# Kernel tuning notes

Hardware: AMD Instinct MI355X
Metric: run time of the kernel (lower is better)

## Reference

```python
import jax, jax.numpy as jnp
import numpy as np

DIM = 2048
N_HEAD = 16

def setup_inputs() -> dict:
    key = jax.random.key(0)
    ks = jax.random.split(key, 5)
    s_in = 1.0 / np.sqrt(DIM)
    x = jax.random.normal(ks[0], (4, 2048, DIM), dtype=jnp.float32)
    W_attn = jax.random.normal(ks[1], (DIM, 3 * DIM), dtype=jnp.float32) * s_in
    b_attn = jnp.zeros((3 * DIM,), dtype=jnp.float32)
    W_proj = jax.random.normal(ks[2], (DIM, DIM), dtype=jnp.float32) * s_in
    b_proj = jnp.zeros((DIM,), dtype=jnp.float32)
    return {"x": x, "W_attn": W_attn, "b_attn": b_attn, "W_proj": W_proj, "b_proj": b_proj}

def reference(x, W_attn, b_attn, W_proj, b_proj):
    B, T, C = x.shape
    H = N_HEAD
    Dh = C // H
    qkv = x @ W_attn + b_attn              # [B,T,3C]
    q, k, v = jnp.split(qkv, 3, axis=-1)
    # [B,T,C] -> [B,H,T,Dh]
    q = q.reshape(B, T, H, Dh).transpose(0, 2, 1, 3)
    k = k.reshape(B, T, H, Dh).transpose(0, 2, 1, 3)
    v = v.reshape(B, T, H, Dh).transpose(0, 2, 1, 3)
    scale = 1.0 / jnp.sqrt(jnp.asarray(Dh, dtype=x.dtype))
    att = jnp.einsum('bhqd,bhkd->bhqk', q, k) * scale
    att = jax.nn.softmax(att, axis=-1)
    y = jnp.einsum('bhqk,bhkd->bhqd', att, v)  # [B,H,T,Dh]
    y = y.transpose(0, 2, 1, 3).reshape(B, T, C)
    y = y @ W_proj + b_proj
    return y
```

## Files before the change

kernel.cpp:

```cpp
#include <hip/hip_runtime.h>


using bhalf  = __bf16;
using bhalf8 = __attribute__((ext_vector_type(8))) __bf16;
using floatx4 = __attribute__((ext_vector_type(4))) float;

#define MFMA16(A, B, C) __builtin_amdgcn_mfma_f32_16x16x32_bf16(A, B, C, 0, 0, 0)

__device__ __forceinline__ void gload16(const void* g, void* l) {
  __builtin_amdgcn_global_load_lds(
      (const __attribute__((address_space(1))) unsigned int*)g,
      (__attribute__((address_space(3))) unsigned int*)l, 16, 0, 0);
}

constexpr int Bn = 4, Tn = 2048, Cn = 2048, Hn = 16, Dh = 128;
constexpr int Kdim = Cn;
constexpr size_t SLOT = (size_t)Hn * Tn * Dh;

__global__ __launch_bounds__(256) void cvt_x(const float* __restrict__ in,
                                             bhalf* __restrict__ out) {
  const size_t i = ((size_t)blockIdx.x * 256 + threadIdx.x) * 8;
  const float4 a = *reinterpret_cast<const float4*>(in + i);
  const float4 b = *reinterpret_cast<const float4*>(in + i + 4);
  bhalf8 v;
  v[0] = (bhalf)a.x; v[1] = (bhalf)a.y; v[2] = (bhalf)a.z; v[3] = (bhalf)a.w;
  v[4] = (bhalf)b.x; v[5] = (bhalf)b.y; v[6] = (bhalf)b.z; v[7] = (bhalf)b.w;
  *reinterpret_cast<bhalf8*>(out + i) = v;
}

__global__ __launch_bounds__(256) void transpose_cvt(const float* __restrict__ in,
                                                     bhalf* __restrict__ out,
                                                     int ldin, int ldout, int coff) {
  __shared__ unsigned short tile[64][65];
  const int c0 = blockIdx.x * 64, r0 = blockIdx.y * 64;
  const int tx = threadIdx.x & 15, ty = threadIdx.x >> 4;
#pragma unroll
  for (int i = 0; i < 4; i++) {
    const int r = ty + i * 16;
    const float4 u = *reinterpret_cast<const float4*>(in + (size_t)(r0 + r) * ldin + coff + c0 + tx * 4);
    tile[r][tx * 4 + 0] = __builtin_bit_cast(unsigned short, (bhalf)u.x);
    tile[r][tx * 4 + 1] = __builtin_bit_cast(unsigned short, (bhalf)u.y);
    tile[r][tx * 4 + 2] = __builtin_bit_cast(unsigned short, (bhalf)u.z);
    tile[r][tx * 4 + 3] = __builtin_bit_cast(unsigned short, (bhalf)u.w);
  }
  __syncthreads();
#pragma unroll
  for (int i = 0; i < 4; i++) {
    const int c = ty + i * 16;
    ushort4 u;
    u.x = tile[tx * 4 + 0][c]; u.y = tile[tx * 4 + 1][c];
    u.z = tile[tx * 4 + 2][c]; u.w = tile[tx * 4 + 3][c];
    *reinterpret_cast<ushort4*>((unsigned short*)out + (size_t)(c0 + c) * ldout + r0 + tx * 4) = u;
  }
}

__global__ __launch_bounds__(256, 3) void gemm_qk(const bhalf* __restrict__ A,
                                                  const bhalf* __restrict__ Bt,
                                                  const float* __restrict__ bias,
                                                  bhalf* __restrict__ oq,
                                                  bhalf* __restrict__ ok) {
  __shared__ __align__(16) bhalf sA[128 * 64];
  __shared__ __align__(16) bhalf sB[128 * 64];
  const int tid = threadIdx.x;
  const int lane = tid & 63, wv = tid >> 6;
  const int ln = lane & 15, quad = lane >> 4;
  const int wr = wv >> 1, wc = wv & 1;
  const int m0 = blockIdx.y * 128, n0 = blockIdx.x * 128;

  const floatx4 fzero = {0.f, 0.f, 0.f, 0.f};
  floatx4 acc[4][4];
#pragma unroll
  for (int i = 0; i < 4; i++)
#pragma unroll
    for (int j = 0; j < 4; j++) acc[i][j] = fzero;

  const int schunk = (lane & 7) ^ ((lane >> 3) & 7);
  const bhalf* aStage = A + (size_t)(m0 + wv * 32 + (lane >> 3)) * Kdim + schunk * 8;
  const bhalf* bStage = Bt + (size_t)(n0 + wv * 32 + (lane >> 3)) * Kdim + schunk * 8;
  bhalf* sAw = &sA[(wv * 32) * 64];
  bhalf* sBw = &sB[(wv * 32) * 64];

  for (int k0 = 0; k0 < Kdim; k0 += 64) {
#pragma unroll
    for (int j = 0; j < 4; j++) gload16(aStage + (size_t)j * 8 * Kdim + k0, sAw + j * 8 * 64);
#pragma unroll
    for (int j = 0; j < 4; j++) gload16(bStage + (size_t)j * 8 * Kdim + k0, sBw + j * 8 * 64);
    __syncthreads();
#pragma unroll
    for (int ks = 0; ks < 2; ks++) {
      bhalf8 af[4], bfr[4];
#pragma unroll
      for (int mi = 0; mi < 4; mi++)
        af[mi] = *reinterpret_cast<const bhalf8*>(
            &sA[(wr * 64 + mi * 16 + ln) * 64 + ((ks * 4 + quad) ^ (ln & 7)) * 8]);
#pragma unroll
      for (int ni = 0; ni < 4; ni++)
        bfr[ni] = *reinterpret_cast<const bhalf8*>(
            &sB[(wc * 64 + ni * 16 + ln) * 64 + ((ks * 4 + quad) ^ (ln & 7)) * 8]);
#pragma unroll
      for (int mi = 0; mi < 4; mi++)
#pragma unroll
        for (int ni = 0; ni < 4; ni++)
          acc[mi][ni] = MFMA16(af[mi], bfr[ni], acc[mi][ni]);
    }
    __syncthreads();
  }

  const int b = m0 >> 11, t0 = m0 & 2047;
  const int which = n0 >> 11;
  const int h = (n0 & 2047) >> 7;
  bhalf* op = which == 0 ? oq : ok;
  float bv[4];
#pragma unroll
  for (int ni = 0; ni < 4; ni++) bv[ni] = bias[n0 + wc * 64 + ni * 16 + ln];
  const size_t base = (size_t)b * (2 * SLOT) + ((size_t)h * Tn + t0) * Dh;
#pragma unroll
  for (int mi = 0; mi < 4; mi++)
#pragma unroll
    for (int ni = 0; ni < 4; ni++)
#pragma unroll
      for (int r = 0; r < 4; r++) {
        const int t = wr * 64 + mi * 16 + quad * 4 + r;
        const int d = wc * 64 + ni * 16 + ln;
        op[base + (size_t)t * Dh + d] = (bhalf)(acc[mi][ni][r] + bv[ni]);
      }
}

template <int MODE>
__global__ __launch_bounds__(256, 3) void gemm_xa(const float* __restrict__ A,
                                                  const bhalf* __restrict__ Bt,
                                                  const float* __restrict__ bias,
                                                  bhalf* __restrict__ oq,
                                                  bhalf* __restrict__ ok) {
  __shared__ __align__(16) float sA[128 * 64];
  __shared__ __align__(16) bhalf sB[128 * 64];
  const int tid = threadIdx.x;
  const int lane = tid & 63, wv = tid >> 6;
  const int ln = lane & 15, quad = lane >> 4;
  const int wr = wv >> 1, wc = wv & 1;
  const int m0 = blockIdx.y * 128, n0 = blockIdx.x * 128;

  const floatx4 fzero = {0.f, 0.f, 0.f, 0.f};
  floatx4 acc[4][4];
#pragma unroll
  for (int i = 0; i < 4; i++)
#pragma unroll
    for (int j = 0; j < 4; j++) acc[i][j] = fzero;

  const int schunkB = (lane & 7) ^ ((lane >> 3) & 7);
  const bhalf* bStage = Bt + (size_t)(n0 + wv * 32 + (lane >> 3)) * Kdim + schunkB * 8;
  bhalf* sBw = &sB[(wv * 32) * 64];
  const int rA = lane >> 4, cA = lane & 15;
  float* sAw = &sA[(wv * 32) * 64];

  for (int k0 = 0; k0 < Kdim; k0 += 64) {
#pragma unroll
    for (int j = 0; j < 8; j++) {
      const int rloc = j * 4 + rA;
      const int gc = cA ^ (rloc & 15);
      gload16(A + (size_t)(m0 + wv * 32 + rloc) * Kdim + k0 + gc * 4, sAw + (j * 4) * 64);
    }
#pragma unroll
    for (int j = 0; j < 4; j++) gload16(bStage + (size_t)j * 8 * Kdim + k0, sBw + j * 8 * 64);
    __syncthreads();
#pragma unroll
    for (int ks = 0; ks < 2; ks++) {
      bhalf8 af[4], bfr[4];
#pragma unroll
      for (int mi = 0; mi < 4; mi++) {
        const int row = wr * 64 + mi * 16 + ln;
        const int c0c = ks * 8 + quad * 2;
        const float4 lo = *reinterpret_cast<const float4*>(&sA[row * 64 + ((c0c ^ ln) * 4)]);
        const float4 hi = *reinterpret_cast<const float4*>(&sA[row * 64 + (((c0c + 1) ^ ln) * 4)]);
        bhalf8 t;
        t[0] = (bhalf)lo.x; t[1] = (bhalf)lo.y; t[2] = (bhalf)lo.z; t[3] = (bhalf)lo.w;
        t[4] = (bhalf)hi.x; t[5] = (bhalf)hi.y; t[6] = (bhalf)hi.z; t[7] = (bhalf)hi.w;
        af[mi] = t;
      }
#pragma unroll
      for (int ni = 0; ni < 4; ni++)
        bfr[ni] = *reinterpret_cast<const bhalf8*>(
            &sB[(wc * 64 + ni * 16 + ln) * 64 + ((ks * 4 + quad) ^ (ln & 7)) * 8]);
#pragma unroll
      for (int i = 0; i < 4; i++)
#pragma unroll
        for (int j = 0; j < 4; j++) {
          if (MODE == 2)
            acc[i][j] = MFMA16(bfr[i], af[j], acc[i][j]);
          else
            acc[i][j] = MFMA16(af[i], bfr[j], acc[i][j]);
        }
    }
    __syncthreads();
  }

  const int b = m0 >> 11, t0 = m0 & 2047;
  if (MODE == 0) {
    const int which = n0 >> 11;
    const int h = (n0 & 2047) >> 7;
    bhalf* op = which == 0 ? oq : ok;
    float bv[4];
#pragma unroll
    for (int ni = 0; ni < 4; ni++) bv[ni] = bias[n0 + wc * 64 + ni * 16 + ln];
    const size_t base = (size_t)b * (2 * SLOT) + ((size_t)h * Tn + t0) * Dh;
#pragma unroll
    for (int mi = 0; mi < 4; mi++)
#pragma unroll
      for (int ni = 0; ni < 4; ni++)
#pragma unroll
        for (int r = 0; r < 4; r++) {
          const int t = wr * 64 + mi * 16 + quad * 4 + r;
          const int d = wc * 64 + ni * 16 + ln;
          op[base + (size_t)t * Dh + d] = (bhalf)(acc[mi][ni][r] + bv[ni]);
        }
  } else {
    const int h = n0 >> 7;
    const size_t base = (size_t)(b * Hn + h) * Dh * Tn;
#pragma unroll
    for (int ni = 0; ni < 4; ni++)
#pragma unroll
      for (int mi = 0; mi < 4; mi++)
#pragma unroll
        for (int r = 0; r < 4; r++) {
          const int d = wc * 64 + ni * 16 + quad * 4 + r;
          const int t = t0 + wr * 64 + mi * 16 + ln;
          oq[base + (size_t)d * Tn + t] = (bhalf)(acc[ni][mi][r] + bias[n0 + d]);
        }
  }
}

__global__ __launch_bounds__(256, 3) void gemm_proj(const bhalf* __restrict__ A,
                                                    const bhalf* __restrict__ Bt,
                                                    const float* __restrict__ bias,
                                                    float* __restrict__ of) {
  __shared__ __align__(16) bhalf sA[128 * 64];
  __shared__ __align__(16) bhalf sB[128 * 64];
  const int tid = threadIdx.x;
  const int lane = tid & 63, wv = tid >> 6;
  const int ln = lane & 15, quad = lane >> 4;
  const int wr = wv >> 1, wc = wv & 1;
  const int m0 = blockIdx.y * 128, n0 = blockIdx.x * 128;

  const floatx4 fzero = {0.f, 0.f, 0.f, 0.f};
  floatx4 acc[4][4];
#pragma unroll
  for (int i = 0; i < 4; i++)
#pragma unroll
    for (int j = 0; j < 4; j++) acc[i][j] = fzero;

  const int schunk = (lane & 7) ^ ((lane >> 3) & 7);
  const bhalf* aStage = A + (size_t)(m0 + wv * 32 + (lane >> 3)) * Kdim + schunk * 8;
  const bhalf* bStage = Bt + (size_t)(n0 + wv * 32 + (lane >> 3)) * Kdim + schunk * 8;
  bhalf* sAw = &sA[(wv * 32) * 64];
  bhalf* sBw = &sB[(wv * 32) * 64];

  for (int k0 = 0; k0 < Kdim; k0 += 64) {
#pragma unroll
    for (int j = 0; j < 4; j++) gload16(aStage + (size_t)j * 8 * Kdim + k0, sAw + j * 8 * 64);
#pragma unroll
    for (int j = 0; j < 4; j++) gload16(bStage + (size_t)j * 8 * Kdim + k0, sBw + j * 8 * 64);
    __syncthreads();
#pragma unroll
    for (int ks = 0; ks < 2; ks++) {
      bhalf8 af[4], bfr[4];
#pragma unroll
      for (int mi = 0; mi < 4; mi++)
        af[mi] = *reinterpret_cast<const bhalf8*>(
            &sA[(wr * 64 + mi * 16 + ln) * 64 + ((ks * 4 + quad) ^ (ln & 7)) * 8]);
#pragma unroll
      for (int ni = 0; ni < 4; ni++)
        bfr[ni] = *reinterpret_cast<const bhalf8*>(
            &sB[(wc * 64 + ni * 16 + ln) * 64 + ((ks * 4 + quad) ^ (ln & 7)) * 8]);
#pragma unroll
      for (int mi = 0; mi < 4; mi++)
#pragma unroll
        for (int ni = 0; ni < 4; ni++)
          acc[mi][ni] = MFMA16(af[mi], bfr[ni], acc[mi][ni]);
    }
    __syncthreads();
  }

  float bv[4];
#pragma unroll
  for (int ni = 0; ni < 4; ni++) bv[ni] = bias[n0 + wc * 64 + ni * 16 + ln];
#pragma unroll
  for (int mi = 0; mi < 4; mi++)
#pragma unroll
    for (int ni = 0; ni < 4; ni++)
#pragma unroll
      for (int r = 0; r < 4; r++) {
        const int row = m0 + wr * 64 + mi * 16 + quad * 4 + r;
        const int col = n0 + wc * 64 + ni * 16 + ln;
        of[(size_t)row * Cn + col] = acc[mi][ni][r] + bv[ni];
      }
}

__global__ __launch_bounds__(256, 4) void flash_attn_all(const bhalf* __restrict__ qk,
                                                         const bhalf* __restrict__ vt,
                                                         bhalf* __restrict__ yb) {
  __shared__ __align__(16) bhalf sK[64 * 128];
  __shared__ __align__(16) bhalf sVT[128 * 64];
  __shared__ __align__(16) bhalf sP[64 * 64];
  const int tid = threadIdx.x;
  const int lane = tid & 63, wv = tid >> 6;
  const int ln = lane & 15, quad = lane >> 4;
  const int rl = lane >> 4, cl = lane & 15;
  const int l = blockIdx.x + (int)gridDim.x * blockIdx.y;
  const int b = l >> 9;
  const int l5 = l & 511;
  const int h = ((l5 & 7) << 1) | ((l5 >> 3) & 1);
  const int t0q = (l5 >> 4) * 64;
  const bhalf* Qb  = qk + (size_t)b * 2 * SLOT;
  const bhalf* Kb  = Qb + SLOT;
  const bhalf* VTb = vt + (size_t)b * SLOT;
  bhalf* Ob        = yb + (size_t)b * SLOT;
  const size_t hb = (size_t)h * Tn * Dh;
  constexpr float kSc = 0.08838834764831845f * 1.4426950408889634f;

  bhalf8 qf[4];
#pragma unroll
  for (int kd = 0; kd < 4; kd++)
    qf[kd] = *reinterpret_cast<const bhalf8*>(
        Qb + hb + (size_t)(t0q + wv * 16 + ln) * Dh + kd * 32 + quad * 8);

  const floatx4 fzero = {0.f, 0.f, 0.f, 0.f};
  floatx4 oAcc[8];
#pragma unroll
  for (int di = 0; di < 8; di++) oAcc[di] = fzero;
  float lrow[4] = {0.f, 0.f, 0.f, 0.f};

  auto stageK = [&](int t0k) {
#pragma unroll
    for (int j = 0; j < 4; j++) {
      const int rloc = wv * 16 + j * 4 + rl;
      const int c = cl ^ (rloc & 15);
      gload16(Kb + hb + (size_t)(t0k + rloc) * Dh + c * 8, sK + (wv * 16 + j * 4) * 128);
    }
  };
  auto stageV = [&](int t0k) {
#pragma unroll
    for (int j = 0; j < 4; j++) {
      const int dloc = j * 32 + wv * 8 + (lane >> 3);
      const int c = (lane & 7) ^ (dloc & 7);
      gload16(VTb + hb + (size_t)dloc * Tn + t0k + c * 8, sVT + (j * 32 + wv * 8) * 64);
    }
  };

  stageK(0);
  asm volatile("" ::: "memory");
  stageV(0);

  for (int t0k = 0; t0k < Tn; t0k += 64) {
    asm volatile("s_waitcnt vmcnt(4)" ::: "memory");
    __builtin_amdgcn_s_barrier();
    asm volatile("" ::: "memory");

    floatx4 sAcc[4];
#pragma unroll
    for (int ni = 0; ni < 4; ni++) sAcc[ni] = fzero;
    __builtin_amdgcn_s_setprio(1);
#pragma unroll
    for (int kd = 0; kd < 4; kd++) {
#pragma unroll
      for (int ni = 0; ni < 4; ni++) {
        const bhalf8 bfr = *reinterpret_cast<const bhalf8*>(
            &sK[(ni * 16 + ln) * 128 + ((kd * 4 + quad) ^ ln) * 8]);
        sAcc[ni] = MFMA16(qf[kd], bfr, sAcc[ni]);
      }
    }
    __builtin_amdgcn_s_setprio(0);

#pragma unroll
    for (int r = 0; r < 4; r++) {
      float rs = 0.f;
#pragma unroll
      for (int ni = 0; ni < 4; ni++) {
        const float p = exp2f(sAcc[ni][r] * kSc);
        sAcc[ni][r] = p;
        rs += p;
      }
      rs += __shfl_xor(rs, 1);
      rs += __shfl_xor(rs, 2);
      rs += __shfl_xor(rs, 4);
      rs += __shfl_xor(rs, 8);
      lrow[r] += rs;
    }

    asm volatile("s_waitcnt vmcnt(0)" ::: "memory");
    __builtin_amdgcn_s_barrier();
    asm volatile("" ::: "memory");
    if (t0k + 64 < Tn) stageK(t0k + 64);

#pragma unroll
    for (int ni = 0; ni < 4; ni++)
#pragma unroll
      for (int r = 0; r < 4; r++) {
        const int qrow = wv * 16 + quad * 4 + r;
        const int kcol = ni * 16 + ln;
        sP[qrow * 64 + (((kcol >> 3) ^ (qrow & 7)) * 8) + (kcol & 7)] =
            (bhalf)sAcc[ni][r];
      }
    asm volatile("s_waitcnt lgkmcnt(0)" ::: "memory");
    __builtin_amdgcn_s_barrier();
    asm volatile("" ::: "memory");

    __builtin_amdgcn_s_setprio(1);
#pragma unroll
    for (int kt = 0; kt < 2; kt++) {
      const bhalf8 ap = *reinterpret_cast<const bhalf8*>(
          &sP[(wv * 16 + ln) * 64 + ((kt * 4 + quad) ^ (ln & 7)) * 8]);
#pragma unroll
      for (int di = 0; di < 8; di++) {
        const bhalf8 bv = *reinterpret_cast<const bhalf8*>(
            &sVT[(di * 16 + ln) * 64 + ((kt * 4 + quad) ^ (ln & 7)) * 8]);
        oAcc[di] = MFMA16(ap, bv, oAcc[di]);
      }
    }
    __builtin_amdgcn_s_setprio(0);

    asm volatile("s_waitcnt lgkmcnt(0)" ::: "memory");
    __builtin_amdgcn_s_barrier();
    asm volatile("" ::: "memory");
    if (t0k + 64 < Tn) stageV(t0k + 64);
  }

#pragma unroll
  for (int r = 0; r < 4; r++) {
    const float inv = 1.0f / lrow[r];
    const int t = t0q + wv * 16 + quad * 4 + r;
    const size_t rowb = (size_t)t * Cn + h * Dh;
#pragma unroll
    for (int di = 0; di < 8; di++)
      Ob[rowb + di * 16 + ln] = (bhalf)(oAcc[di][r] * inv);
  }
}

extern "C" void kernel_launch(void* const* d_in, const int* in_sizes, int n_in,
                              void* d_out, int out_size, void* d_ws, size_t ws_size,
                              hipStream_t stream) {
  const float* x      = (const float*)d_in[0];
  const float* W_attn = (const float*)d_in[1];
  const float* b_attn = (const float*)d_in[2];
  const float* W_proj = (const float*)d_in[3];
  const float* b_proj = (const float*)d_in[4];
  float* out = (float*)d_out;
  bhalf* ws  = (bhalf*)d_ws;

  bhalf* xb   = ws;
  bhalf* wtQK = ws + 4 * SLOT;
  bhalf* wtV  = ws;
  bhalf* vt   = ws + 2 * SLOT;
  bhalf* y    = ws;
  bhalf* wtP  = ws + 4 * SLOT;
  bhalf* qk   = (bhalf*)d_out;

  cvt_x<<<8192, 256, 0, stream>>>(x, xb);

  transpose_cvt<<<dim3(64, 32), 256, 0, stream>>>(W_attn, wtQK, 3 * Cn, Kdim, 0);
  gemm_qk<<<dim3(32, 64), 256, 0, stream>>>(xb, wtQK, b_attn, qk, qk + SLOT);

  transpose_cvt<<<dim3(32, 32), 256, 0, stream>>>(W_attn, wtV, 3 * Cn, Kdim, 2 * Cn);
  gemm_xa<2><<<dim3(16, 64), 256, 0, stream>>>(x, wtV, b_attn + 2 * Cn, vt, nullptr);

  flash_attn_all<<<dim3(32, 64), 256, 0, stream>>>(qk, vt, y);

  transpose_cvt<<<dim3(32, 32), 256, 0, stream>>>(W_proj, wtP, Kdim, Kdim, 0);
  gemm_proj<<<dim3(16, 64), 256, 0, stream>>>(y, wtP, b_proj, out);
}
```

Before: 751.4 us.

## Double query tile per attention block to reuse K/V tiles, split launch

The flash attention kernel now processes 128 query rows per block (32 per wave, two MFMA row groups) instead of 64, so each staged K and V^T tile feeds twice as many MFMAs and global K/V traffic is halved. One barrier before the P·V step is removed, since each wave now reads only its own P rows. The grid shrinks to 512 blocks per launch, issued as two launches covering two batches each. Occupancy drops (launch bounds 3, larger sP buffer, more accumulator registers), and gemm_qk's launch bound changes from 3 to 4.

```diff
diff --git a/kernel.cpp b/kernel.cpp
--- a/kernel.cpp
+++ b/kernel.cpp
@@ -54,7 +54,7 @@
   }
 }
 
-__global__ __launch_bounds__(256, 3) void gemm_qk(const bhalf* __restrict__ A,
+__global__ __launch_bounds__(256, 4) void gemm_qk(const bhalf* __restrict__ A,
                                                   const bhalf* __restrict__ Bt,
                                                   const float* __restrict__ bias,
                                                   bhalf* __restrict__ oq,
@@ -295,21 +295,21 @@
       }
 }
 
-__global__ __launch_bounds__(256, 4) void flash_attn_all(const bhalf* __restrict__ qk,
-                                                         const bhalf* __restrict__ vt,
-                                                         bhalf* __restrict__ yb) {
+__global__ __launch_bounds__(256, 3) void flash_attn2(const bhalf* __restrict__ qk,
+                                                      const bhalf* __restrict__ vt,
+                                                      bhalf* __restrict__ yb) {
   __shared__ __align__(16) bhalf sK[64 * 128];
   __shared__ __align__(16) bhalf sVT[128 * 64];
-  __shared__ __align__(16) bhalf sP[64 * 64];
+  __shared__ __align__(16) bhalf sP[128 * 64];
   const int tid = threadIdx.x;
   const int lane = tid & 63, wv = tid >> 6;
   const int ln = lane & 15, quad = lane >> 4;
   const int rl = lane >> 4, cl = lane & 15;
-  const int l = blockIdx.x + (int)gridDim.x * blockIdx.y;
-  const int b = l >> 9;
-  const int l5 = l & 511;
+  const int l = blockIdx.x;
+  const int b = l >> 8;
+  const int l5 = l & 255;
   const int h = ((l5 & 7) << 1) | ((l5 >> 3) & 1);
-  const int t0q = (l5 >> 4) * 64;
+  const int t0q = (l5 >> 4) * 128;
   const bhalf* Qb  = qk + (size_t)b * 2 * SLOT;
   const bhalf* Kb  = Qb + SLOT;
   const bhalf* VTb = vt + (size_t)b * SLOT;
@@ -317,17 +317,21 @@
   const size_t hb = (size_t)h * Tn * Dh;
   constexpr float kSc = 0.08838834764831845f * 1.4426950408889634f;
 
-  bhalf8 qf[4];
-#pragma unroll
-  for (int kd = 0; kd < 4; kd++)
-    qf[kd] = *reinterpret_cast<const bhalf8*>(
-        Qb + hb + (size_t)(t0q + wv * 16 + ln) * Dh + kd * 32 + quad * 8);
+  bhalf8 qf[2][4];
+#pragma unroll
+  for (int mi = 0; mi < 2; mi++)
+#pragma unroll
+    for (int kd = 0; kd < 4; kd++)
+      qf[mi][kd] = *reinterpret_cast<const bhalf8*>(
+          Qb + hb + (size_t)(t0q + wv * 32 + mi * 16 + ln) * Dh + kd * 32 + quad * 8);
 
   const floatx4 fzero = {0.f, 0.f, 0.f, 0.f};
-  floatx4 oAcc[8];
-#pragma unroll
-  for (int di = 0; di < 8; di++) oAcc[di] = fzero;
-  float lrow[4] = {0.f, 0.f, 0.f, 0.f};
+  floatx4 oAcc[2][8];
+#pragma unroll
+  for (int mi = 0; mi < 2; mi++)
+#pragma unroll
+    for (int di = 0; di < 8; di++) oAcc[mi][di] = fzero;
+  float lrow[2][4] = {{0.f, 0.f, 0.f, 0.f}, {0.f, 0.f, 0.f, 0.f}};
 
   auto stageK = [&](int t0k) {
 #pragma unroll
@@ -355,9 +359,11 @@
     __builtin_amdgcn_s_barrier();
     asm volatile("" ::: "memory");
 
-    floatx4 sAcc[4];
-#pragma unroll
-    for (int ni = 0; ni < 4; ni++) sAcc[ni] = fzero;
+    floatx4 sAcc[2][4];
+#pragma unroll
+    for (int mi = 0; mi < 2; mi++)
+#pragma unroll
+      for (int ni = 0; ni < 4; ni++) sAcc[mi][ni] = fzero;
     __builtin_amdgcn_s_setprio(1);
 #pragma unroll
     for (int kd = 0; kd < 4; kd++) {
@@ -365,26 +371,29 @@
       for (int ni = 0; ni < 4; ni++) {
         const bhalf8 bfr = *reinterpret_cast<const bhalf8*>(
             &sK[(ni * 16 + ln) * 128 + ((kd * 4 + quad) ^ ln) * 8]);
-        sAcc[ni] = MFMA16(qf[kd], bfr, sAcc[ni]);
+        sAcc[0][ni] = MFMA16(qf[0][kd], bfr, sAcc[0][ni]);
+        sAcc[1][ni] = MFMA16(qf[1][kd], bfr, sAcc[1][ni]);
       }
     }
     __builtin_amdgcn_s_setprio(0);
 
 #pragma unroll
-    for (int r = 0; r < 4; r++) {
-      float rs = 0.f;
-#pragma unroll
-      for (int ni = 0; ni < 4; ni++) {
-        const float p = exp2f(sAcc[ni][r] * kSc);
-        sAcc[ni][r] = p;
-        rs += p;
-      }
-      rs += __shfl_xor(rs, 1);
-      rs += __shfl_xor(rs, 2);
-      rs += __shfl_xor(rs, 4);
-      rs += __shfl_xor(rs, 8);
-      lrow[r] += rs;
-    }
+    for (int mi = 0; mi < 2; mi++)
+#pragma unroll
+      for (int r = 0; r < 4; r++) {
+        float rs = 0.f;
+#pragma unroll
+        for (int ni = 0; ni < 4; ni++) {
+          const float p = exp2f(sAcc[mi][ni][r] * kSc);
+          sAcc[mi][ni][r] = p;
+          rs += p;
+        }
+        rs += __shfl_xor(rs, 1);
+        rs += __shfl_xor(rs, 2);
+        rs += __shfl_xor(rs, 4);
+        rs += __shfl_xor(rs, 8);
+        lrow[mi][r] += rs;
+      }
 
     asm volatile("s_waitcnt vmcnt(0)" ::: "memory");
     __builtin_amdgcn_s_barrier();
@@ -392,28 +401,32 @@
     if (t0k + 64 < Tn) stageK(t0k + 64);
 
 #pragma unroll
-    for (int ni = 0; ni < 4; ni++)
-#pragma unroll
-      for (int r = 0; r < 4; r++) {
-        const int qrow = wv * 16 + quad * 4 + r;
-        const int kcol = ni * 16 + ln;
-        sP[qrow * 64 + (((kcol >> 3) ^ (qrow & 7)) * 8) + (kcol & 7)] =
-            (bhalf)sAcc[ni][r];
-      }
+    for (int mi = 0; mi < 2; mi++)
+#pragma unroll
+      for (int ni = 0; ni < 4; ni++)
+#pragma unroll
+        for (int r = 0; r < 4; r++) {
+          const int qrow = wv * 32 + mi * 16 + quad * 4 + r;
+          const int kcol = ni * 16 + ln;
+          sP[qrow * 64 + (((kcol >> 3) ^ (qrow & 7)) * 8) + (kcol & 7)] =
+              (bhalf)sAcc[mi][ni][r];
+        }
     asm volatile("s_waitcnt lgkmcnt(0)" ::: "memory");
-    __builtin_amdgcn_s_barrier();
-    asm volatile("" ::: "memory");
 
     __builtin_amdgcn_s_setprio(1);
 #pragma unroll
     for (int kt = 0; kt < 2; kt++) {
-      const bhalf8 ap = *reinterpret_cast<const bhalf8*>(
-          &sP[(wv * 16 + ln) * 64 + ((kt * 4 + quad) ^ (ln & 7)) * 8]);
+      bhalf8 ap[2];
+#pragma unroll
+      for (int mi = 0; mi < 2; mi++)
+        ap[mi] = *reinterpret_cast<const bhalf8*>(
+            &sP[(wv * 32 + mi * 16 + ln) * 64 + ((kt * 4 + quad) ^ (ln & 7)) * 8]);
 #pragma unroll
       for (int di = 0; di < 8; di++) {
         const bhalf8 bv = *reinterpret_cast<const bhalf8*>(
             &sVT[(di * 16 + ln) * 64 + ((kt * 4 + quad) ^ (ln & 7)) * 8]);
-        oAcc[di] = MFMA16(ap, bv, oAcc[di]);
+        oAcc[0][di] = MFMA16(ap[0], bv, oAcc[0][di]);
+        oAcc[1][di] = MFMA16(ap[1], bv, oAcc[1][di]);
       }
     }
     __builtin_amdgcn_s_setprio(0);
@@ -425,14 +438,16 @@
   }
 
 #pragma unroll
-  for (int r = 0; r < 4; r++) {
-    const float inv = 1.0f / lrow[r];
-    const int t = t0q + wv * 16 + quad * 4 + r;
-    const size_t rowb = (size_t)t * Cn + h * Dh;
-#pragma unroll
-    for (int di = 0; di < 8; di++)
-      Ob[rowb + di * 16 + ln] = (bhalf)(oAcc[di][r] * inv);
-  }
+  for (int mi = 0; mi < 2; mi++)
+#pragma unroll
+    for (int r = 0; r < 4; r++) {
+      const float inv = 1.0f / lrow[mi][r];
+      const int t = t0q + wv * 32 + mi * 16 + quad * 4 + r;
+      const size_t rowb = (size_t)t * Cn + h * Dh;
+#pragma unroll
+      for (int di = 0; di < 8; di++)
+        Ob[rowb + di * 16 + ln] = (bhalf)(oAcc[mi][di][r] * inv);
+    }
 }
 
 extern "C" void kernel_launch(void* const* d_in, const int* in_sizes, int n_in,
@@ -462,7 +477,8 @@
   transpose_cvt<<<dim3(32, 32), 256, 0, stream>>>(W_attn, wtV, 3 * Cn, Kdim, 2 * Cn);
   gemm_xa<2><<<dim3(16, 64), 256, 0, stream>>>(x, wtV, b_attn + 2 * Cn, vt, nullptr);
 
-  flash_attn_all<<<dim3(32, 64), 256, 0, stream>>>(qk, vt, y);
+  flash_attn2<<<512, 256, 0, stream>>>(qk, vt, y);
+  flash_attn2<<<512, 256, 0, stream>>>(qk + 4 * SLOT, vt + 2 * SLOT, y + 2 * SLOT);
 
   transpose_cvt<<<dim3(32, 32), 256, 0, stream>>>(W_proj, wtP, Kdim, Kdim, 0);
   gemm_proj<<<dim3(16, 64), 256, 0, stream>>>(y, wtP, b_proj, out);
```

Result: slower. 1.398 ms (+86.1%).
